# Kernel tuning notes

Hardware: AMD Instinct MI355X
Metric: run time of the kernel (lower is better)

Reference implementation:

```python
import jax, jax.numpy as jnp
import numpy as np

DIM = 512
CODEBOOK_SIZE = 1024
BETA = 0.25


def setup_inputs() -> dict:
    key = jax.random.key(0)
    k1, k2 = jax.random.split(key)
    B, T = 16, 2048
    z = jax.random.normal(k1, (B, DIM, T), dtype=jnp.float32)
    # torch init: uniform_(-1/codebook_size, 1/codebook_size)
    codebook = jax.random.uniform(
        k2, (CODEBOOK_SIZE, DIM), dtype=jnp.float32,
        minval=-1.0 / CODEBOOK_SIZE, maxval=1.0 / CODEBOOK_SIZE)
    return {"z": z, "codebook": codebook}


def reference(z, codebook):
    B, D, T = z.shape
    z_flat = jnp.transpose(z, (0, 2, 1)).reshape(-1, D)  # [N, D], N = B*T
    # Squared euclidean distances (argmin identical to cdist argmin):
    # |z|^2 - 2 z.W^T + |w|^2
    z_sq = jnp.sum(z_flat * z_flat, axis=-1, keepdims=True)          # [N, 1]
    w_sq = jnp.sum(codebook * codebook, axis=-1)                     # [K]
    dist2 = z_sq - 2.0 * jnp.einsum('nd,kd->nk', z_flat, codebook) + w_sq
    indices_flat = jnp.argmin(dist2, axis=-1)                        # [N]
    z_q_flat = codebook[indices_flat]                                # [N, D]
    z_q = jnp.transpose(z_q_flat.reshape(B, T, D), (0, 2, 1))        # [B, D, T]
    # Straight-through estimator
    z_q_st = z + jax.lax.stop_gradient(z_q - z)
    commitment_loss = jnp.mean((jax.lax.stop_gradient(z_q) - z) ** 2)
    codebook_loss = jnp.mean((z_q - jax.lax.stop_gradient(z)) ** 2)
    loss = commitment_loss + BETA * codebook_loss
    indices = indices_flat.reshape(B, T)
    return (z_q_st, indices, loss)
```

## Files before the change

kernel.cpp:

```cpp
#include <hip/hip_runtime.h>

typedef _Float16 f16_t;
typedef _Float16 f16x8 __attribute__((ext_vector_type(8)));
typedef float    f32x4 __attribute__((ext_vector_type(4)));

#define DIMD 512
#define KCB  1024
#define TT   2048
#define BB   16
#define NTOT (BB*TT)
#define OUT_IDX  (BB*DIMD*TT)
#define OUT_LOSS (OUT_IDX + NTOT)
#define TAU 3.0e-4f
#define NEG2_SCALE (-0.001953125f)
#define BTOK 64

__device__ __forceinline__ void gll16(const f16_t* g, f16_t* l) {
    __builtin_amdgcn_global_load_lds(
        (const __attribute__((address_space(1))) unsigned int*)g,
        (__attribute__((address_space(3))) unsigned int*)l, 16, 0, 0);
}

__global__ __launch_bounds__(256) void prep_kernel(const float* __restrict__ cb,
                                                   f16_t* __restrict__ wf,
                                                   float* __restrict__ w2,
                                                   float* __restrict__ cbT) {
    const int wave = threadIdx.x >> 6, lane = threadIdx.x & 63;
    const int row  = blockIdx.x * 4 + wave;
    const float* src = cb + (size_t)row * DIMD + lane * 8;
    float4 v0 = *(const float4*)(src);
    float4 v1 = *(const float4*)(src + 4);
    f16x8 o;
    o[0] = (f16_t)(v0.x * 1024.f); o[1] = (f16_t)(v0.y * 1024.f);
    o[2] = (f16_t)(v0.z * 1024.f); o[3] = (f16_t)(v0.w * 1024.f);
    o[4] = (f16_t)(v1.x * 1024.f); o[5] = (f16_t)(v1.y * 1024.f);
    o[6] = (f16_t)(v1.z * 1024.f); o[7] = (f16_t)(v1.w * 1024.f);
    *(f16x8*)(wf + (size_t)row * DIMD + lane * 8) = o;
    float vals[8] = {v0.x, v0.y, v0.z, v0.w, v1.x, v1.y, v1.z, v1.w};
    #pragma unroll
    for (int u = 0; u < 8; ++u)
        cbT[(size_t)(lane * 8 + u) * KCB + row] = vals[u];
    float s0 = v0.x * v0.x, s1 = v0.y * v0.y, s2 = v0.z * v0.z, s3 = v0.w * v0.w;
    float s4 = v1.x * v1.x, s5 = v1.y * v1.y, s6 = v1.z * v1.z, s7 = v1.w * v1.w;
    double s = (double)s0 + (double)s1 + (double)s2 + (double)s3 +
               (double)s4 + (double)s5 + (double)s6 + (double)s7;
    #pragma unroll
    for (int m = 1; m < 64; m <<= 1) s += __shfl_xor(s, m, 64);
    if (lane == 0) w2[row] = (float)s;
}

__global__ __launch_bounds__(256, 2) void fast_kernel(
    const float* __restrict__ z, const f16_t* __restrict__ wf,
    const float* __restrict__ w2, float* __restrict__ out_idx_f,
    float* __restrict__ score, float* __restrict__ z2,
    int* __restrict__ cnt, int* __restrict__ list)
{
    extern __shared__ __align__(16) char smem[];
    f16_t* As = (f16_t*)smem;
    f16_t* Bs = (f16_t*)(smem + (64 << 10));

    const int tid  = threadIdx.x;
    const int wave = tid >> 6;
    const int lane = tid & 63;
    const int m    = lane & 15;
    const int quad = lane >> 4;
    const int rh   = wave & 1;
    const int chh  = wave >> 1;
    const int tok0 = blockIdx.x * BTOK;

    double zp;
    {
        const int tok = tok0 + lane;
        const int b = tok >> 11, t = tok & 2047;
        const float* src = z + (size_t)b * DIMD * TT + t;
        const int d0 = wave * 128;
        zp = 0.0;
        f16_t* arow = As + lane * DIMD;
        const int x7 = lane & 7;
        for (int j = 0; j < 16; ++j) {
            f16x8 o;
            #pragma unroll
            for (int u = 0; u < 8; ++u) {
                float v = src[(size_t)(d0 + j * 8 + u) * TT];
                o[u] = (f16_t)v;
                float vv = v * v;
                zp += (double)vv;
            }
            *(f16x8*)(arow + (((wave * 16 + j) ^ x7) * 8)) = o;
        }
    }
    float* zredp = (float*)(Bs + 4096);
    zredp[wave * 64 + lane] = (float)zp;

    const f16_t* gB[2]; f16_t* lB[2];
    #pragma unroll
    for (int q = 0; q < 2; ++q) {
        int s = q * 256 + tid;
        int row = s >> 2, p = s & 3;
        gB[q] = wf + (size_t)row * DIMD + (p ^ ((row >> 1) & 3)) * 8;
        lB[q] = Bs + s * 8;
    }
    gll16(gB[0], lB[0]);
    gll16(gB[1], lB[1]);
    __syncthreads();

    if (wave == 0)
        z2[tok0 + lane] = ((zredp[lane] + zredp[64 + lane]) + zredp[128 + lane])
                          + zredp[192 + lane];
    __syncthreads();

    float b1[8], b2[8]; int i1[8];
    #pragma unroll
    for (int r = 0; r < 8; ++r) { b1[r] = 3.4e38f; b2[r] = 3.4e38f; i1[r] = 0; }

    const int a7 = m & 7;
    const f16_t* Arow0 = As + (rh * 32 + m) * DIMD;
    const int bq = (quad ^ ((m >> 1) & 3)) * 8;
    const int br = chh * 64 + m;

    for (int ct = 0; ct < 8; ++ct) {
        f32x4 acc[2][4] = {};
        #pragma unroll
        for (int dcc = 0; dcc < 16; ++dcc) {
            const int n = ct * 16 + dcc;
            if (n + 1 < 128) {
                const int nct = (n + 1) >> 4, ndc = (n + 1) & 15;
                const size_t off = (size_t)nct * (128 * DIMD) + (size_t)ndc * 32;
                const int wb = (n + 1) & 1;
                gll16(gB[0] + off, lB[0] + wb * 4096);
                gll16(gB[1] + off, lB[1] + wb * 4096);
            }
            {
                const f16_t* Bc = Bs + (n & 1) * 4096;
                const int aswz = ((dcc * 4 + quad) ^ a7) * 8;
                f16x8 af0 = *(const f16x8*)(Arow0 + aswz);
                f16x8 af1 = *(const f16x8*)(Arow0 + 16 * DIMD + aswz);
                f16x8 bf0 = *(const f16x8*)(Bc + (br +  0) * 32 + bq);
                f16x8 bf1 = *(const f16x8*)(Bc + (br + 16) * 32 + bq);
                f16x8 bf2 = *(const f16x8*)(Bc + (br + 32) * 32 + bq);
                f16x8 bf3 = *(const f16x8*)(Bc + (br + 48) * 32 + bq);
                __builtin_amdgcn_s_setprio(1);
                acc[0][0] = __builtin_amdgcn_mfma_f32_16x16x32_f16(af0, bf0, acc[0][0], 0, 0, 0);
                acc[0][1] = __builtin_amdgcn_mfma_f32_16x16x32_f16(af0, bf1, acc[0][1], 0, 0, 0);
                acc[0][2] = __builtin_amdgcn_mfma_f32_16x16x32_f16(af0, bf2, acc[0][2], 0, 0, 0);
                acc[0][3] = __builtin_amdgcn_mfma_f32_16x16x32_f16(af0, bf3, acc[0][3], 0, 0, 0);
                acc[1][0] = __builtin_amdgcn_mfma_f32_16x16x32_f16(af1, bf0, acc[1][0], 0, 0, 0);
                acc[1][1] = __builtin_amdgcn_mfma_f32_16x16x32_f16(af1, bf1, acc[1][1], 0, 0, 0);
                acc[1][2] = __builtin_amdgcn_mfma_f32_16x16x32_f16(af1, bf2, acc[1][2], 0, 0, 0);
                acc[1][3] = __builtin_amdgcn_mfma_f32_16x16x32_f16(af1, bf3, acc[1][3], 0, 0, 0);
                __builtin_amdgcn_s_setprio(0);
            }
            __syncthreads();
        }
        #pragma unroll
        for (int nt = 0; nt < 4; ++nt) {
            const int col = ct * 128 + chh * 64 + nt * 16 + m;
            const float w2c = w2[col];
            #pragma unroll
            for (int mt = 0; mt < 2; ++mt)
                #pragma unroll
                for (int r = 0; r < 4; ++r) {
                    float s = fmaf(NEG2_SCALE, acc[mt][nt][r], w2c);
                    const int ri = mt * 4 + r;
                    if (s < b1[ri]) { b2[ri] = b1[ri]; b1[ri] = s; i1[ri] = col; }
                    else if (s < b2[ri]) b2[ri] = s;
                }
        }
    }

    #pragma unroll
    for (int msk = 1; msk < 16; msk <<= 1) {
        #pragma unroll
        for (int ri = 0; ri < 8; ++ri) {
            float o1 = __shfl_xor(b1[ri], msk, 64);
            int   oi = __shfl_xor(i1[ri], msk, 64);
            float o2 = __shfl_xor(b2[ri], msk, 64);
            if (o1 < b1[ri] || (o1 == b1[ri] && oi < i1[ri])) {
                b2[ri] = fminf(b1[ri], o2); b1[ri] = o1; i1[ri] = oi;
            } else {
                b2[ri] = fminf(b2[ri], o1);
            }
        }
    }

    float* Lb1 = (float*)As;
    float* Lb2 = Lb1 + 64;
    int*   Li  = (int*)(Lb2 + 64);
    if (chh == 1 && m == 0) {
        #pragma unroll
        for (int ri = 0; ri < 8; ++ri) {
            int row = rh * 32 + (ri >> 2) * 16 + quad * 4 + (ri & 3);
            Lb1[row] = b1[ri]; Lb2[row] = b2[ri]; Li[row] = i1[ri];
        }
    }
    __syncthreads();
    if (chh == 0 && m == 0) {
        #pragma unroll
        for (int ri = 0; ri < 8; ++ri) {
            int row = rh * 32 + (ri >> 2) * 16 + quad * 4 + (ri & 3);
            float o1 = Lb1[row], o2 = Lb2[row]; int oi = Li[row];
            if (o1 < b1[ri] || (o1 == b1[ri] && oi < i1[ri])) {
                b2[ri] = fminf(b1[ri], o2); b1[ri] = o1; i1[ri] = oi;
            } else {
                b2[ri] = fminf(b2[ri], o1);
            }
            int tok = tok0 + row;
            out_idx_f[tok] = (float)i1[ri];
            score[tok] = b1[ri];
            if (b2[ri] - b1[ri] <= TAU) {
                int p = atomicAdd(cnt, 1);
                list[p] = tok;
            }
        }
    }
}

__global__ __launch_bounds__(256) void recheck_kernel(
    const float* __restrict__ z, const float* __restrict__ cbT,
    const float* __restrict__ w2, const int* __restrict__ cnt,
    const int* __restrict__ list, float* __restrict__ out_idx_f)
{
    __shared__ float zrow[4][DIMD];
    __shared__ float z2s[4];
    __shared__ float rv[4][4];
    __shared__ int   ri[4][4];

    const int tid  = threadIdx.x;
    const int wave = tid >> 6;
    const int lane = tid & 63;
    const int total = *cnt;
    const int ngrp = (total + 3) >> 2;
    const int k0 = tid * 4;

    for (int g = blockIdx.x; g < ngrp; g += gridDim.x) {
        __syncthreads();
        const int nrows = min(4, total - g * 4);
        {
            int idx = g * 4 + wave;
            int tok = (idx < total) ? list[idx] : list[g * 4];
            int b = tok >> 11, t = tok & 2047;
            const float* zb = z + (size_t)b * DIMD * TT + t;
            double zp = 0.0;
            #pragma unroll
            for (int j = 0; j < 8; ++j) {
                int d = lane + 64 * j;
                float v = zb[(size_t)d * TT];
                zrow[wave][d] = v;
                float vv = v * v;
                zp += (double)vv;
            }
            #pragma unroll
            for (int msk = 1; msk < 64; msk <<= 1) zp += __shfl_xor(zp, msk, 64);
            if (lane == 0) z2s[wave] = (float)zp;
        }
        __syncthreads();

        double acc[4][4] = {};
        f32x4 cw0 = *(const f32x4*)(cbT + (size_t)0 * KCB + k0);
        f32x4 cw1 = *(const f32x4*)(cbT + (size_t)1 * KCB + k0);
        f32x4 cw2 = *(const f32x4*)(cbT + (size_t)2 * KCB + k0);
        f32x4 cw3 = *(const f32x4*)(cbT + (size_t)3 * KCB + k0);
        for (int d = 0; d < DIMD; d += 4) {
            f32x4 n0, n1, n2, n3;
            if (d + 4 < DIMD) {
                n0 = *(const f32x4*)(cbT + (size_t)(d + 4) * KCB + k0);
                n1 = *(const f32x4*)(cbT + (size_t)(d + 5) * KCB + k0);
                n2 = *(const f32x4*)(cbT + (size_t)(d + 6) * KCB + k0);
                n3 = *(const f32x4*)(cbT + (size_t)(d + 7) * KCB + k0);
            }
            #pragma unroll
            for (int r = 0; r < 4; ++r) {
                f32x4 zv = *(const f32x4*)&zrow[r][d];
                #pragma unroll
                for (int j = 0; j < 4; ++j) {
                    acc[r][j] = fma((double)zv[0], (double)cw0[j], acc[r][j]);
                    acc[r][j] = fma((double)zv[1], (double)cw1[j], acc[r][j]);
                    acc[r][j] = fma((double)zv[2], (double)cw2[j], acc[r][j]);
                    acc[r][j] = fma((double)zv[3], (double)cw3[j], acc[r][j]);
                }
            }
            cw0 = n0; cw1 = n1; cw2 = n2; cw3 = n3;
        }

        f32x4 w2q = *(const f32x4*)(w2 + k0);
        float bv[4]; int bi[4];
        #pragma unroll
        for (int r = 0; r < 4; ++r) { bv[r] = 3.4e38f; bi[r] = 0; }
        #pragma unroll
        for (int r = 0; r < 4; ++r)
            #pragma unroll
            for (int j = 0; j < 4; ++j) {
                float dotf = (float)acc[r][j];
                float t2   = z2s[r] - 2.0f * dotf;
                float s    = t2 + w2q[j];
                if (s < bv[r]) { bv[r] = s; bi[r] = k0 + j; }
            }
        #pragma unroll
        for (int msk = 1; msk < 64; msk <<= 1) {
            #pragma unroll
            for (int r = 0; r < 4; ++r) {
                float ov = __shfl_xor(bv[r], msk, 64);
                int   oi = __shfl_xor(bi[r], msk, 64);
                if (ov < bv[r] || (ov == bv[r] && oi < bi[r])) { bv[r] = ov; bi[r] = oi; }
            }
        }
        if (lane == 0) {
            #pragma unroll
            for (int r = 0; r < 4; ++r) { rv[wave][r] = bv[r]; ri[wave][r] = bi[r]; }
        }
        __syncthreads();
        if (tid < nrows) {
            float v = rv[0][tid]; int k = ri[0][tid];
            #pragma unroll
            for (int w = 1; w < 4; ++w) {
                if (rv[w][tid] < v || (rv[w][tid] == v && ri[w][tid] < k)) {
                    v = rv[w][tid]; k = ri[w][tid];
                }
            }
            out_idx_f[list[g * 4 + tid]] = (float)k;
        }
    }
}

__global__ __launch_bounds__(256) void gather_kernel(
    const float* __restrict__ cb, const float* __restrict__ idx_f,
    float* __restrict__ out)
{
    const size_t base = ((size_t)blockIdx.x * 256 + threadIdx.x) * 4;
    const int t  = (int)(base % TT);
    const int bd = (int)(base / TT);
    const int d  = bd & (DIMD - 1);
    const int b  = bd >> 9;

    const float* ip = idx_f + b * TT + t;
    int k0 = (int)(ip[0] + 0.5f);
    int k1 = (int)(ip[1] + 0.5f);
    int k2 = (int)(ip[2] + 0.5f);
    int k3 = (int)(ip[3] + 0.5f);
    float4 ov = make_float4(cb[(size_t)k0 * DIMD + d],
                            cb[(size_t)k1 * DIMD + d],
                            cb[(size_t)k2 * DIMD + d],
                            cb[(size_t)k3 * DIMD + d]);
    *(float4*)(out + base) = ov;
}

__global__ __launch_bounds__(256) void loss_kernel(const float* __restrict__ z2,
                                                   const float* __restrict__ score,
                                                   float* __restrict__ loss)
{
    __shared__ double red[4];
    const int idx = blockIdx.x * 1024 + threadIdx.x * 4;
    float4 a = *(const float4*)(z2 + idx);
    float4 s = *(const float4*)(score + idx);
    double part = ((double)a.x + (double)s.x) + ((double)a.y + (double)s.y) +
                  ((double)a.z + (double)s.z) + ((double)a.w + (double)s.w);
    #pragma unroll
    for (int m = 1; m < 64; m <<= 1) part += __shfl_xor(part, m, 64);
    const int lane = threadIdx.x & 63, wv = threadIdx.x >> 6;
    if (lane == 0) red[wv] = part;
    __syncthreads();
    if (threadIdx.x == 0) {
        double tot = red[0] + red[1] + red[2] + red[3];
        atomicAdd(loss, (float)(tot * (1.25 / (double)(BB * DIMD * TT))));
    }
}

extern "C" void kernel_launch(void* const* d_in, const int* in_sizes, int n_in,
                              void* d_out, int out_size, void* d_ws, size_t ws_size,
                              hipStream_t stream) {
    const float* z  = (const float*)d_in[0];
    const float* cb = (const float*)d_in[1];
    float* out = (float*)d_out;

    float* cbT = (float*)((char*)out + (33u << 20));

    char* wsb = (char*)d_ws;
    f16_t* wf    = (f16_t*)wsb;
    float* w2    = (float*)(wsb + (1 << 20));
    int*   cnt   = (int*)(wsb + (1 << 20) + 4096);
    int*   list  = (int*)(wsb + (1 << 20) + 8192);
    float* z2    = (float*)(wsb + (1 << 20) + 8192 + (128 << 10));
    float* score = z2 + NTOT;

    hipMemsetAsync(out + OUT_LOSS, 0, sizeof(float), stream);
    hipMemsetAsync(cnt, 0, sizeof(int), stream);
    prep_kernel<<<KCB / 4, 256, 0, stream>>>(cb, wf, w2, cbT);
    fast_kernel<<<NTOT / BTOK, 256, 80 << 10, stream>>>(
        z, wf, w2, out + OUT_IDX, score, z2, cnt, list);
    recheck_kernel<<<512, 256, 0, stream>>>(z, cbT, w2, cnt, list, out + OUT_IDX);
    gather_kernel<<<(BB * DIMD * TT) / (256 * 4), 256, 0, stream>>>(
        cb, out + OUT_IDX, out);
    loss_kernel<<<NTOT / 1024, 256, 0, stream>>>(z2, score, out + OUT_LOSS);
}
```

Baseline: 321.9 us.

## Transpose codebook gather through LDS, fuse loss reduction, widen recheck blocks

The gather kernel now has each block handle 64 tokens. It reads whole codebook rows with vectorized loads and transposes them through padded shared memory, so the [B,D,T] output is written with coalesced float4 stores instead of scattered per-element codebook reads. The loss reduction is folded into the first 32 gather blocks, which removes one kernel launch. The recheck kernel moves to 512 threads handling 8 tokens per group with 2 codewords per thread, so each codebook load is reused across more rows. The trade-off is about 133KB of dynamic LDS per gather block, which limits occupancy.

Result: faster. 280.7 us (-12.8%).

```diff
diff --git a/kernel.cpp b/kernel.cpp
--- a/kernel.cpp
+++ b/kernel.cpp
@@ -3,6 +3,7 @@
 typedef _Float16 f16_t;
 typedef _Float16 f16x8 __attribute__((ext_vector_type(8)));
 typedef float    f32x4 __attribute__((ext_vector_type(4)));
+typedef float    f32x2 __attribute__((ext_vector_type(2)));
 
 #define DIMD 512
 #define KCB  1024
@@ -215,29 +216,29 @@
     }
 }
 
-__global__ __launch_bounds__(256) void recheck_kernel(
+__global__ __launch_bounds__(512) void recheck_kernel(
     const float* __restrict__ z, const float* __restrict__ cbT,
     const float* __restrict__ w2, const int* __restrict__ cnt,
     const int* __restrict__ list, float* __restrict__ out_idx_f)
 {
-    __shared__ float zrow[4][DIMD];
-    __shared__ float z2s[4];
-    __shared__ float rv[4][4];
-    __shared__ int   ri[4][4];
+    __shared__ float zrow[8][DIMD];
+    __shared__ float z2s[8];
+    __shared__ float rv[8][8];
+    __shared__ int   ri[8][8];
 
     const int tid  = threadIdx.x;
     const int wave = tid >> 6;
     const int lane = tid & 63;
     const int total = *cnt;
-    const int ngrp = (total + 3) >> 2;
-    const int k0 = tid * 4;
+    const int ngrp = (total + 7) >> 3;
+    const int k0 = tid * 2;
 
     for (int g = blockIdx.x; g < ngrp; g += gridDim.x) {
         __syncthreads();
-        const int nrows = min(4, total - g * 4);
+        const int nrows = min(8, total - g * 8);
         {
-            int idx = g * 4 + wave;
-            int tok = (idx < total) ? list[idx] : list[g * 4];
+            int idx = g * 8 + wave;
+            int tok = (idx < total) ? list[idx] : list[g * 8];
             int b = tok >> 11, t = tok & 2047;
             const float* zb = z + (size_t)b * DIMD * TT + t;
             double zp = 0.0;
@@ -255,24 +256,24 @@
         }
         __syncthreads();
 
-        double acc[4][4] = {};
-        f32x4 cw0 = *(const f32x4*)(cbT + (size_t)0 * KCB + k0);
-        f32x4 cw1 = *(const f32x4*)(cbT + (size_t)1 * KCB + k0);
-        f32x4 cw2 = *(const f32x4*)(cbT + (size_t)2 * KCB + k0);
-        f32x4 cw3 = *(const f32x4*)(cbT + (size_t)3 * KCB + k0);
+        double acc[8][2] = {};
+        f32x2 cw0 = *(const f32x2*)(cbT + (size_t)0 * KCB + k0);
+        f32x2 cw1 = *(const f32x2*)(cbT + (size_t)1 * KCB + k0);
+        f32x2 cw2 = *(const f32x2*)(cbT + (size_t)2 * KCB + k0);
+        f32x2 cw3 = *(const f32x2*)(cbT + (size_t)3 * KCB + k0);
         for (int d = 0; d < DIMD; d += 4) {
-            f32x4 n0, n1, n2, n3;
+            f32x2 n0, n1, n2, n3;
             if (d + 4 < DIMD) {
-                n0 = *(const f32x4*)(cbT + (size_t)(d + 4) * KCB + k0);
-                n1 = *(const f32x4*)(cbT + (size_t)(d + 5) * KCB + k0);
-                n2 = *(const f32x4*)(cbT + (size_t)(d + 6) * KCB + k0);
-                n3 = *(const f32x4*)(cbT + (size_t)(d + 7) * KCB + k0);
-            }
-            #pragma unroll
-            for (int r = 0; r < 4; ++r) {
+                n0 = *(const f32x2*)(cbT + (size_t)(d + 4) * KCB + k0);
+                n1 = *(const f32x2*)(cbT + (size_t)(d + 5) * KCB + k0);
+                n2 = *(const f32x2*)(cbT + (size_t)(d + 6) * KCB + k0);
+                n3 = *(const f32x2*)(cbT + (size_t)(d + 7) * KCB + k0);
+            }
+            #pragma unroll
+            for (int r = 0; r < 8; ++r) {
                 f32x4 zv = *(const f32x4*)&zrow[r][d];
                 #pragma unroll
-                for (int j = 0; j < 4; ++j) {
+                for (int j = 0; j < 2; ++j) {
                     acc[r][j] = fma((double)zv[0], (double)cw0[j], acc[r][j]);
                     acc[r][j] = fma((double)zv[1], (double)cw1[j], acc[r][j]);
                     acc[r][j] = fma((double)zv[2], (double)cw2[j], acc[r][j]);
@@ -282,14 +283,14 @@
             cw0 = n0; cw1 = n1; cw2 = n2; cw3 = n3;
         }
 
-        f32x4 w2q = *(const f32x4*)(w2 + k0);
-        float bv[4]; int bi[4];
-        #pragma unroll
-        for (int r = 0; r < 4; ++r) { bv[r] = 3.4e38f; bi[r] = 0; }
-        #pragma unroll
-        for (int r = 0; r < 4; ++r)
-            #pragma unroll
-            for (int j = 0; j < 4; ++j) {
+        f32x2 w2q = *(const f32x2*)(w2 + k0);
+        float bv[8]; int bi[8];
+        #pragma unroll
+        for (int r = 0; r < 8; ++r) { bv[r] = 3.4e38f; bi[r] = 0; }
+        #pragma unroll
+        for (int r = 0; r < 8; ++r)
+            #pragma unroll
+            for (int j = 0; j < 2; ++j) {
                 float dotf = (float)acc[r][j];
                 float t2   = z2s[r] - 2.0f * dotf;
                 float s    = t2 + w2q[j];
@@ -298,7 +299,7 @@
         #pragma unroll
         for (int msk = 1; msk < 64; msk <<= 1) {
             #pragma unroll
-            for (int r = 0; r < 4; ++r) {
+            for (int r = 0; r < 8; ++r) {
                 float ov = __shfl_xor(bv[r], msk, 64);
                 int   oi = __shfl_xor(bi[r], msk, 64);
                 if (ov < bv[r] || (ov == bv[r] && oi < bi[r])) { bv[r] = ov; bi[r] = oi; }
@@ -306,62 +307,81 @@
         }
         if (lane == 0) {
             #pragma unroll
-            for (int r = 0; r < 4; ++r) { rv[wave][r] = bv[r]; ri[wave][r] = bi[r]; }
+            for (int r = 0; r < 8; ++r) { rv[wave][r] = bv[r]; ri[wave][r] = bi[r]; }
         }
         __syncthreads();
-        if (tid < nrows) {
+        if (tid < 8) {
             float v = rv[0][tid]; int k = ri[0][tid];
             #pragma unroll
-            for (int w = 1; w < 4; ++w) {
+            for (int w = 1; w < 8; ++w) {
                 if (rv[w][tid] < v || (rv[w][tid] == v && ri[w][tid] < k)) {
                     v = rv[w][tid]; k = ri[w][tid];
                 }
             }
-            out_idx_f[list[g * 4 + tid]] = (float)k;
-        }
-    }
-}
-
+            if (tid < nrows) out_idx_f[list[g * 8 + tid]] = (float)k;
+        }
+    }
+}
+
+#define GLDS_BYTES (512 * 65 * 4 + 256)
 __global__ __launch_bounds__(256) void gather_kernel(
     const float* __restrict__ cb, const float* __restrict__ idx_f,
-    float* __restrict__ out)
+    const float* __restrict__ z2, const float* __restrict__ score,
+    float* __restrict__ out, float* __restrict__ loss)
 {
-    const size_t base = ((size_t)blockIdx.x * 256 + threadIdx.x) * 4;
-    const int t  = (int)(base % TT);
-    const int bd = (int)(base / TT);
-    const int d  = bd & (DIMD - 1);
-    const int b  = bd >> 9;
-
-    const float* ip = idx_f + b * TT + t;
-    int k0 = (int)(ip[0] + 0.5f);
-    int k1 = (int)(ip[1] + 0.5f);
-    int k2 = (int)(ip[2] + 0.5f);
-    int k3 = (int)(ip[3] + 0.5f);
-    float4 ov = make_float4(cb[(size_t)k0 * DIMD + d],
-                            cb[(size_t)k1 * DIMD + d],
-                            cb[(size_t)k2 * DIMD + d],
-                            cb[(size_t)k3 * DIMD + d]);
-    *(float4*)(out + base) = ov;
-}
-
-__global__ __launch_bounds__(256) void loss_kernel(const float* __restrict__ z2,
-                                                   const float* __restrict__ score,
-                                                   float* __restrict__ loss)
-{
-    __shared__ double red[4];
-    const int idx = blockIdx.x * 1024 + threadIdx.x * 4;
-    float4 a = *(const float4*)(z2 + idx);
-    float4 s = *(const float4*)(score + idx);
-    double part = ((double)a.x + (double)s.x) + ((double)a.y + (double)s.y) +
-                  ((double)a.z + (double)s.z) + ((double)a.w + (double)s.w);
-    #pragma unroll
-    for (int m = 1; m < 64; m <<= 1) part += __shfl_xor(part, m, 64);
-    const int lane = threadIdx.x & 63, wv = threadIdx.x >> 6;
-    if (lane == 0) red[wv] = part;
+    extern __shared__ __align__(16) char gsm[];
+    float* zqT = (float*)gsm;
+    int*   ki  = (int*)(gsm + 512 * 65 * 4);
+
+    const int tid  = threadIdx.x;
+    const int wave = tid >> 6, lane = tid & 63;
+    const int tok0 = blockIdx.x * 64;
+    const int bidx = tok0 >> 11;
+    const int t0   = tok0 & 2047;
+
+    if (tid < 64) ki[tid] = (int)(idx_f[tok0 + tid] + 0.5f);
     __syncthreads();
-    if (threadIdx.x == 0) {
-        double tot = red[0] + red[1] + red[2] + red[3];
-        atomicAdd(loss, (float)(tot * (1.25 / (double)(BB * DIMD * TT))));
+
+    for (int jj = 0; jj < 16; ++jj) {
+        const int j = wave * 16 + jj;
+        const float* crow = cb + (size_t)ki[j] * DIMD;
+        #pragma unroll
+        for (int seg = 0; seg < 2; ++seg) {
+            const int d = seg * 256 + lane * 4;
+            f32x4 v = *(const f32x4*)(crow + d);
+            zqT[(d + 0) * 65 + j] = v[0];
+            zqT[(d + 1) * 65 + j] = v[1];
+            zqT[(d + 2) * 65 + j] = v[2];
+            zqT[(d + 3) * 65 + j] = v[3];
+        }
+    }
+    __syncthreads();
+
+    float* obase = out + (size_t)bidx * DIMD * TT + t0;
+    for (int it = 0; it < 32; ++it) {
+        const int d  = it * 16 + (tid >> 4);
+        const int j4 = (tid & 15) * 4;
+        const float* zr = &zqT[d * 65 + j4];
+        f32x4 v; v[0] = zr[0]; v[1] = zr[1]; v[2] = zr[2]; v[3] = zr[3];
+        *(f32x4*)(obase + (size_t)d * TT + j4) = v;
+    }
+
+    if (blockIdx.x < 32) {
+        __syncthreads();
+        double* red = (double*)gsm;
+        const int idx = blockIdx.x * 1024 + tid * 4;
+        float4 a = *(const float4*)(z2 + idx);
+        float4 s = *(const float4*)(score + idx);
+        double part = ((double)a.x + (double)s.x) + ((double)a.y + (double)s.y) +
+                      ((double)a.z + (double)s.z) + ((double)a.w + (double)s.w);
+        #pragma unroll
+        for (int mm = 1; mm < 64; mm <<= 1) part += __shfl_xor(part, mm, 64);
+        if (lane == 0) red[wave] = part;
+        __syncthreads();
+        if (tid == 0) {
+            double tot = red[0] + red[1] + red[2] + red[3];
+            atomicAdd(loss, (float)(tot * (1.25 / (double)(BB * DIMD * TT))));
+        }
     }
 }
 
@@ -387,8 +407,7 @@
     prep_kernel<<<KCB / 4, 256, 0, stream>>>(cb, wf, w2, cbT);
     fast_kernel<<<NTOT / BTOK, 256, 80 << 10, stream>>>(
         z, wf, w2, out + OUT_IDX, score, z2, cnt, list);
-    recheck_kernel<<<512, 256, 0, stream>>>(z, cbT, w2, cnt, list, out + OUT_IDX);
-    gather_kernel<<<(BB * DIMD * TT) / (256 * 4), 256, 0, stream>>>(
-        cb, out + OUT_IDX, out);
-    loss_kernel<<<NTOT / 1024, 256, 0, stream>>>(z2, score, out + OUT_LOSS);
-}
+    recheck_kernel<<<512, 512, 0, stream>>>(z, cbT, w2, cnt, list, out + OUT_IDX);
+    gather_kernel<<<NTOT / 64, 256, GLDS_BYTES, stream>>>(
+        cb, out + OUT_IDX, z2, score, out, out + OUT_LOSS);
+}
```
